# Kernel tuning notes

Hardware: AMD Instinct MI355X
Metric: run time of the kernel (lower is better)

## Reference

```python
import jax, jax.numpy as jnp
import numpy as np

P = 512       # person_attrs_dim
Z = 4096      # num_zones
T = 16384     # number of timesteps
E = 65536     # number of edges
PENALTY = 10.0


def setup_inputs() -> dict:
    key = jax.random.key(0)
    ks = jax.random.split(key, 10)
    person_attrs = jax.random.normal(ks[0], (P,), dtype=jnp.float32)
    times = jax.random.uniform(ks[1], (T,), dtype=jnp.float32)
    zone_features = jax.random.normal(ks[2], (Z, 16), dtype=jnp.float32)
    edge_index = jax.random.randint(ks[3], (2, E), 0, Z, dtype=jnp.int64)
    s = 0.05
    W1 = jax.random.normal(ks[4], (P + 1, 128), dtype=jnp.float32) * s
    b1 = jnp.zeros((128,), jnp.float32)
    W2 = jax.random.normal(ks[5], (128, 64), dtype=jnp.float32) * s
    b2 = jnp.zeros((64,), jnp.float32)
    W3 = jax.random.normal(ks[6], (64, Z), dtype=jnp.float32) * s
    b3 = jnp.zeros((Z,), jnp.float32)
    return {
        "person_attrs": person_attrs, "times": times,
        "zone_features": zone_features, "edge_index": edge_index,
        "W1": W1, "b1": b1, "W2": W2, "b2": b2, "W3": W3, "b3": b3,
    }


def reference(person_attrs, times, zone_features, edge_index, W1, b1, W2, b2, W3, b3):
    Zn = W3.shape[1]
    Tn = times.shape[0]

    # ---- set_graph_data: symmetric adjacency + self loops ----
    adj = jnp.zeros((Zn, Zn), jnp.float32)
    adj = adj.at[edge_index[0], edge_index[1]].set(1.0)
    adj = adj.at[edge_index[1], edge_index[0]].set(1.0)
    diag = jnp.arange(Zn)
    adj = adj.at[diag, diag].set(1.0)

    # ---- batched MLP over all timesteps (inputs don't depend on decode state) ----
    # input per step: concat(person_attrs, time)  -> [T, P+1]
    x = jnp.concatenate(
        [jnp.broadcast_to(person_attrs, (Tn, person_attrs.shape[0])), times[:, None]],
        axis=1,
    )
    h = jax.nn.relu(x @ W1 + b1)          # [T, 128]  (dropout is identity in eval)
    h = jax.nn.relu(h @ W2 + b2)          # [T, 64]
    raw = h @ W3 + b3                     # [T, Z]

    # ---- sequential graph-masked decode (training=True soft-penalty branch) ----
    def step(cur_zone, raw_t):
        constrained = raw_t - PENALTY * (1.0 - adj[cur_zone])  # [Z]
        nxt = jnp.argmax(constrained).astype(jnp.int32)
        return nxt, constrained

    _, zone_logits = jax.lax.scan(step, jnp.int32(0), raw)     # [T, Z]
    return zone_logits
```

## Files before the change

### kernel.cpp

```cpp
#include <hip/hip_runtime.h>
#include <hip/hip_bf16.h>
#include <stdint.h>

typedef uint16_t u16;
typedef uint32_t u32;
typedef uint64_t u64;
typedef unsigned char u8;

#define TT 16384
#define ZZ 4096
#define EE 65536
#define LBLK 32
#define NBLK 512
#define SUPW 16
#define NSUP 32
#define ADJ_STRIDE 80
#define UCAP 2048
#define PEN 10.0f

#define WS_BITS   0x000000
#define WS_GMKEY  0x200000
#define WS_DEG    0x220000
#define WS_ADJL   0x224000
#define WS_NCH    0x2C4000
#define WS_CVEC   0x2C5000
#define WS_WVEC   0x2C5200
#define WS_H2     0x2C5400
#define WS_M      WS_H2
#define WS_H      0x6C5400
#define WS_SB     0x705400
#define WS_CUR    0x705C00

__device__ __forceinline__ u64 mkkey(float v, u32 z) {
  u32 u = __float_as_uint(v);
  u32 sf = u ^ ((u32)((int)u >> 31) | 0x80000000u);
  return ((u64)sf << 12) | (u64)(4095u - z);
}
__device__ __forceinline__ float key_val(u64 k) {
  u32 sf = (u32)(k >> 12);
  u32 u = (sf & 0x80000000u) ? (sf ^ 0x80000000u) : ~sf;
  return __uint_as_float(u);
}

__device__ __forceinline__ u64 eval_part(int s, int part, const u64* keys, u64 gkey,
                                         const u16* adjl, int nc) {
  const u64* alq = (const u64*)(adjl + (size_t)s * ADJ_STRIDE) + part * 5;
  int cnt = nc - part * 5;
  u64 c0 = (cnt > 0) ? alq[0] : 0;
  u64 c1 = (cnt > 1) ? alq[1] : 0;
  u64 c2 = (cnt > 2) ? alq[2] : 0;
  u64 c3 = (cnt > 3) ? alq[3] : 0;
  u64 c4 = (cnt > 4) ? alq[4] : 0;
  u64 bb = gkey;
#define CM(cv, cnd) { u32 lo = (u32)(cv), hi = (u32)((cv) >> 32);                \
    u64 k0 = keys[lo & 0xFFFFu]; u64 k1 = keys[lo >> 16];                        \
    u64 k2 = keys[hi & 0xFFFFu]; u64 k3 = keys[hi >> 16];                        \
    u64 t01 = k0 > k1 ? k0 : k1; u64 t23 = k2 > k3 ? k2 : k3;                    \
    u64 tm = t01 > t23 ? t01 : t23;                                              \
    if ((cnd) && tm > bb) bb = tm; }
  CM(c0, cnt > 0) CM(c1, cnt > 1) CM(c2, cnt > 2) CM(c3, cnt > 3) CM(c4, cnt > 4)
#undef CM
  return bb;
}

__global__ __launch_bounds__(256) void k_setupA(u32* bits, u32* deg, u16* adjl,
                                                const float* pa, const float* W1,
                                                const float* b1,
                                                float* cvec, float* wvec) {
  __shared__ float pal[512];
  int tid = threadIdx.x;
  if (blockIdx.x < 16) {
    int z = blockIdx.x * 256 + tid;
    bits[(size_t)z * 128 + (z >> 5)] = 1u << (z & 31);
    deg[z] = 1;
    adjl[(size_t)z * ADJ_STRIDE] = (u16)z;
    return;
  }
  for (int i = tid; i < 512; i += 256) pal[i] = pa[i];
  __syncthreads();
  if (tid < 128) {
    float acc = b1[tid];
    for (int i = 0; i < 512; i++) acc = fmaf(pal[i], W1[(size_t)i * 128 + tid], acc);
    cvec[tid] = acc;
    wvec[tid] = W1[512 * 128 + tid];
  }
}

__global__ void k_edges(const int* ei, u32* bits, u32* deg, u16* adjl) {
  int e = blockIdx.x * blockDim.x + threadIdx.x;
  if (e >= EE) return;
  int u = ei[e], v = ei[EE + e];
#pragma unroll
  for (int dir = 0; dir < 2; dir++) {
    int a = dir ? v : u, b = dir ? u : v;
    u32 bit = 1u << (b & 31);
    u32 old = atomicOr(&bits[(size_t)a * 128 + (b >> 5)], bit);
    if (!(old & bit)) {
      u32 p = atomicAdd(&deg[a], 1u);
      if (p < ADJ_STRIDE) adjl[(size_t)a * ADJ_STRIDE + p] = (u16)b;
    }
  }
}

__global__ __launch_bounds__(256) void k_setupC(const u32* deg, u16* adjl, u8* nchp,
                                                const float* times, const float* W2,
                                                const float* b2, const float* cvec,
                                                const float* wvec, float* h2) {
  __shared__ float W2T[64][132];
  __shared__ float h1b[4][128];
  __shared__ float cl[128], wl[128], b2l[64];
  int tid = threadIdx.x;
  if (blockIdx.x < 16) {
    int z = blockIdx.x * 256 + tid;
    int d = (int)deg[z]; if (d > ADJ_STRIDE) d = ADJ_STRIDE;
    int dp = (d + 3) & ~3;
    for (int k = d; k < dp; k++) adjl[(size_t)z * ADJ_STRIDE + k] = (u16)z;
    nchp[z] = (u8)(dp >> 2);
    return;
  }
  for (int idx = tid; idx < 128 * 64; idx += 256) {
    int i = idx >> 6, j = idx & 63;
    W2T[j][i] = W2[idx];
  }
  if (tid < 128) { cl[tid] = cvec[tid]; wl[tid] = wvec[tid]; }
  else if (tid < 192) b2l[tid - 128] = b2[tid - 128];
  __syncthreads();
  int w = tid >> 6, lane = tid & 63;
  int t = (blockIdx.x - 16) * 4 + w;
  float tv = times[t];
  h1b[w][lane]      = fmaxf(fmaf(tv, wl[lane],      cl[lane]),      0.f);
  h1b[w][lane + 64] = fmaxf(fmaf(tv, wl[lane + 64], cl[lane + 64]), 0.f);
  __syncthreads();
  float acc = b2l[lane];
  const float4* hr = (const float4*)&h1b[w][0];
  const float4* Wr = (const float4*)&W2T[lane][0];
#pragma unroll
  for (int i4 = 0; i4 < 32; i4++) {
    float4 a = hr[i4], bb = Wr[i4];
    acc += a.x * bb.x; acc += a.y * bb.y; acc += a.z * bb.z; acc += a.w * bb.w;
  }
  acc = fmaxf(acc, 0.f);
  h2[(size_t)t * 64 + lane] = acc;
}

__global__ __launch_bounds__(256) void k_raw(const float* h2, const float* W3,
                                             const float* b3, float* out,
                                             u64* gmkey) {
  __shared__ float w3t[64][128];
  __shared__ float h2t[64][72];
  int tid = threadIdx.x;
  int zblk = blockIdx.x & 31, tblk = blockIdx.x >> 5;
  int z0 = zblk * 128, t0 = tblk * 64;
#pragma unroll
  for (int it = 0; it < 8; it++) {
    int f4 = tid + it * 256;
    int k = f4 >> 5, jj = (f4 & 31) * 4;
    *(float4*)&w3t[k][jj] = *(const float4*)(W3 + (size_t)k * ZZ + z0 + jj);
  }
#pragma unroll
  for (int it = 0; it < 4; it++) {
    int f4 = tid + it * 256;
    int r = f4 >> 4, kk = (f4 & 15) * 4;
    float4 h = *(const float4*)(h2 + (size_t)(t0 + r) * 64 + kk);
    h2t[kk + 0][r] = h.x; h2t[kk + 1][r] = h.y;
    h2t[kk + 2][r] = h.z; h2t[kk + 3][r] = h.w;
  }
  __syncthreads();
  int zq = tid & 31, tq = tid >> 5;
  float4 acc[8];
#pragma unroll
  for (int r = 0; r < 8; r++) acc[r] = make_float4(0.f, 0.f, 0.f, 0.f);
  for (int k = 0; k < 64; k++) {
    float4 w = *(const float4*)&w3t[k][zq * 4];
    float4 hA = *(const float4*)&h2t[k][tq * 8];
    float4 hB = *(const float4*)&h2t[k][tq * 8 + 4];
    acc[0].x += hA.x * w.x; acc[0].y += hA.x * w.y; acc[0].z += hA.x * w.z; acc[0].w += hA.x * w.w;
    acc[1].x += hA.y * w.x; acc[1].y += hA.y * w.y; acc[1].z += hA.y * w.z; acc[1].w += hA.y * w.w;
    acc[2].x += hA.z * w.x; acc[2].y += hA.z * w.y; acc[2].z += hA.z * w.z; acc[2].w += hA.z * w.w;
    acc[3].x += hA.w * w.x; acc[3].y += hA.w * w.y; acc[3].z += hA.w * w.z; acc[3].w += hA.w * w.w;
    acc[4].x += hB.x * w.x; acc[4].y += hB.x * w.y; acc[4].z += hB.x * w.z; acc[4].w += hB.x * w.w;
    acc[5].x += hB.y * w.x; acc[5].y += hB.y * w.y; acc[5].z += hB.y * w.z; acc[5].w += hB.y * w.w;
    acc[6].x += hB.z * w.x; acc[6].y += hB.z * w.y; acc[6].z += hB.z * w.z; acc[6].w += hB.z * w.w;
    acc[7].x += hB.w * w.x; acc[7].y += hB.w * w.y; acc[7].z += hB.w * w.z; acc[7].w += hB.w * w.w;
  }
  int z = z0 + zq * 4;
  float4 b3v = *(const float4*)(b3 + z);
  int lane = tid & 63;
  int half = lane >> 5;
#pragma unroll
  for (int r = 0; r < 8; r++) {
    int t = t0 + tq * 8 + r;
    float4 v;
    v.x = acc[r].x + b3v.x - PEN; v.y = acc[r].y + b3v.y - PEN;
    v.z = acc[r].z + b3v.z - PEN; v.w = acc[r].w + b3v.w - PEN;
    *(float4*)(out + (size_t)t * ZZ + z) = v;
    float lv = v.x; u32 lz = (u32)z;
    if (v.y > lv) { lv = v.y; lz = (u32)(z + 1); }
    if (v.z > lv) { lv = v.z; lz = (u32)(z + 2); }
    if (v.w > lv) { lv = v.w; lz = (u32)(z + 3); }
    float mv = lv;
#pragma unroll
    for (int off = 16; off >= 1; off >>= 1) {
      float o = __shfl_xor(mv, off);
      mv = o > mv ? o : mv;
    }
    u64 msk = __ballot(lv == mv);
    u32 hm = (u32)(msk >> (half * 32));
    int fl = __ffs(hm) - 1 + half * 32;
    u32 zbest = __shfl(lz, fl);
    if ((lane & 31) == 0)
      atomicMax((unsigned long long*)&gmkey[t], (unsigned long long)mkkey(mv, zbest));
  }
}

__global__ __launch_bounds__(512) void k_stage1(const float* raw, const u16* adjl,
                                                const u8* nchp, const u64* gmkey,
                                                u16* M) {
  __shared__ u64 keys[ZZ];
  __shared__ u16 I[ZZ];
  __shared__ u16 ev[ZZ];
  __shared__ u16 U[2][UCAP];
  __shared__ u8  nchl[ZZ];
  __shared__ u32 markw[128];
  __shared__ u32 mcnt2[2];
  __shared__ u64 gmk[LBLK];
  int tid = threadIdx.x;
  int b = blockIdx.x, t0 = b * LBLK;
  *(u64*)&nchl[tid * 8] = *(const u64*)(nchp + tid * 8);
  if (tid < LBLK) gmk[tid] = gmkey[t0 + tid];
  {
    const float4* src = (const float4*)(raw + (size_t)t0 * ZZ);
    float4 r0 = src[tid], r1 = src[tid + 512];
    int z0 = tid * 4;
    keys[z0 + 0] = mkkey(r0.x, z0 + 0);
    keys[z0 + 1] = mkkey(r0.y, z0 + 1);
    keys[z0 + 2] = mkkey(r0.z, z0 + 2);
    keys[z0 + 3] = mkkey(r0.w, z0 + 3);
    int z1 = (tid + 512) * 4;
    keys[z1 + 0] = mkkey(r1.x, z1 + 0);
    keys[z1 + 1] = mkkey(r1.y, z1 + 1);
    keys[z1 + 2] = mkkey(r1.z, z1 + 2);
    keys[z1 + 3] = mkkey(r1.w, z1 + 3);
  }
  __syncthreads();
  int lane = tid & 63;
  u64 lmask = (((u64)1) << lane) - 1ull;
  int part = tid & 3;
  int m = ZZ, pb = 0;
  bool dense = true;
  for (int i = 0; i < LBLK; i++) {
    int t = t0 + i;
    int tn = t + 1; if (tn > TT - 1) tn = TT - 1;
    const float4* srcn = (const float4*)(raw + (size_t)tn * ZZ);
    float4 p0 = srcn[tid], p1 = srcn[tid + 512];
    if (tid < 128) markw[tid] = 0;
    if (tid == 128) mcnt2[pb ^ 1] = 0;
    u64 gk = gmk[i];
    float gv = key_val(gk) - PEN;
    u32 gi = 4095u - (u32)(gk & 0xFFFu);
    u64 gkey = mkkey(gv, gi);
    int m4 = m << 2;
    for (int u = tid; u < m4; u += 512) {
      int s = dense ? (u >> 2) : (int)U[pb][u >> 2];
      u64 pk = eval_part(s, part, keys, gkey, adjl, (int)nchl[s]);
      u64 o1 = __shfl_xor(pk, 1); pk = o1 > pk ? o1 : pk;
      u64 o2 = __shfl_xor(pk, 2); pk = o2 > pk ? o2 : pk;
      if (part == 0) ev[s] = (u16)(4095u - ((u32)pk & 0xFFFu));
    }
    __syncthreads();
    if (i == 0) {
#pragma unroll
      for (int q = 0; q < 8; q++) {
        int j = tid + q * 512;
        I[j] = ev[j];
      }
    } else {
#pragma unroll
      for (int q = 0; q < 8; q++) {
        int j = tid + q * 512;
        I[j] = ev[I[j]];
      }
    }
    for (int u = tid; u < m; u += 512) {
      int s = dense ? u : (int)U[pb][u];
      u32 ns = ev[s];
      u32 wi = ns >> 5, bit = 1u << (ns & 31);
      u32 old = atomicOr(&markw[wi], bit);
      bool isnew = !(old & bit);
      u64 msk = __ballot(isnew ? 1 : 0);
      u32 base = 0;
      if (lane == 0) base = msk ? atomicAdd(&mcnt2[pb ^ 1], (u32)__popcll(msk)) : 0u;
      base = __shfl(base, 0);
      if (isnew) {
        u32 idx = base + (u32)__popcll(msk & lmask);
        if (idx < UCAP) U[pb ^ 1][idx] = (u16)ns;
      }
    }
    {
      int z0 = tid * 4;
      keys[z0 + 0] = mkkey(p0.x, z0 + 0);
      keys[z0 + 1] = mkkey(p0.y, z0 + 1);
      keys[z0 + 2] = mkkey(p0.z, z0 + 2);
      keys[z0 + 3] = mkkey(p0.w, z0 + 3);
      int z1 = (tid + 512) * 4;
      keys[z1 + 0] = mkkey(p1.x, z1 + 0);
      keys[z1 + 1] = mkkey(p1.y, z1 + 1);
      keys[z1 + 2] = mkkey(p1.z, z1 + 2);
      keys[z1 + 3] = mkkey(p1.w, z1 + 3);
    }
    __syncthreads();
    m = (int)mcnt2[pb ^ 1];
    dense = (m > UCAP);
    if (dense) m = ZZ;
    pb ^= 1;
  }
  {
    u64* md = (u64*)(M + (size_t)b * ZZ);
    md[tid * 2]     = *(const u64*)&I[tid * 8];
    md[tid * 2 + 1] = *(const u64*)&I[tid * 8 + 4];
  }
}

__global__ __launch_bounds__(256) void k_super(const u16* G, u16* H) {
  int g = blockIdx.x, tid = threadIdx.x;
  u32 v[16];
#pragma unroll
  for (int q = 0; q < 16; q++) v[q] = G[(size_t)(g * SUPW) * ZZ + tid + q * 256];
  for (int k = 1; k < SUPW; k++) {
    const u16* Gk = G + (size_t)(g * SUPW + k) * ZZ;
#pragma unroll
    for (int q = 0; q < 16; q++) v[q] = Gk[v[q]];
  }
#pragma unroll
  for (int q = 0; q < 16; q++) H[(size_t)g * ZZ + tid + q * 256] = (u16)v[q];
}

__global__ void k_chase(const u16* G, const u16* H, u32* sb) {
  __shared__ u32 ug[NSUP];
  int tid = threadIdx.x;
  if (tid == 0) {
    u32 s = 0;
    for (int g = 0; g < NSUP; g++) { ug[g] = s; s = H[(size_t)g * ZZ + s]; }
  }
  __syncthreads();
  if (tid < NSUP) {
    u32 s = ug[tid];
    for (int k = 0; k < SUPW; k++) {
      int b = tid * SUPW + k;
      sb[b] = s;
      s = G[(size_t)b * ZZ + s];
    }
  }
}

__global__ __launch_bounds__(64) void k_replay2(const float* out, const u16* adjl,
                                                const u8* nchp, const u64* gmkey,
                                                const u32* sb, u32* curz) {
  int b = blockIdx.x, t0 = b * LBLK;
  int lane = threadIdx.x;
  u32 s = sb[b];
  for (int i = 0; i < LBLK; i++) {
    int t = t0 + i;
    if (lane == 0) curz[t] = s;
    u64 gk = gmkey[t];
    float gv = key_val(gk) - PEN;
    u32 gi = 4095u - (u32)(gk & 0xFFFu);
    int dp = ((int)nchp[s]) << 2;
    const u16* al = adjl + (size_t)s * ADJ_STRIDE;
    const float* r = out + (size_t)t * ZZ;
    float bv = gv; u32 bi = gi;
    if (lane < dp) {
      u32 nb = al[lane]; float v = r[nb];
      if (v > bv || (v == bv && nb < bi)) { bv = v; bi = nb; }
    }
    if (lane + 64 < dp) {
      u32 nb = al[lane + 64]; float v = r[nb];
      if (v > bv || (v == bv && nb < bi)) { bv = v; bi = nb; }
    }
#pragma unroll
    for (int off = 32; off >= 1; off >>= 1) {
      float ov = __shfl_xor(bv, off);
      u32 oi  = __shfl_xor(bi, off);
      if (ov > bv || (ov == bv && oi < bi)) { bv = ov; bi = oi; }
    }
    s = bi;
  }
}

__global__ __launch_bounds__(256) void k_out2(float* out, const u32* curz, const u32* bits) {
  int t = blockIdx.x * 4 + (threadIdx.x >> 6);
  int lane = threadIdx.x & 63;
  u32 c = curz[t];
  u64 w = ((const u64*)(bits + (size_t)c * 128))[lane];
  float* p = out + (size_t)t * ZZ + lane * 64;
  while (w) {
    int bpos = __ffsll((unsigned long long)w) - 1;
    p[bpos] += PEN;
    w &= w - 1;
  }
}

extern "C" void kernel_launch(void* const* d_in, const int* in_sizes, int n_in,
                              void* d_out, int out_size, void* d_ws, size_t ws_size,
                              hipStream_t stream) {
  const float* pa    = (const float*)d_in[0];
  const float* times = (const float*)d_in[1];
  const int*   ei    = (const int*)d_in[3];
  const float* W1    = (const float*)d_in[4];
  const float* b1    = (const float*)d_in[5];
  const float* W2    = (const float*)d_in[6];
  const float* b2    = (const float*)d_in[7];
  const float* W3    = (const float*)d_in[8];
  const float* b3    = (const float*)d_in[9];
  float* out = (float*)d_out;
  char* ws = (char*)d_ws;

  u32* bits = (u32*)(ws + WS_BITS);
  u64* gmkey = (u64*)(ws + WS_GMKEY);
  u32* deg  = (u32*)(ws + WS_DEG);
  u16* adjl = (u16*)(ws + WS_ADJL);
  u8*  nchp = (u8*)(ws + WS_NCH);
  float* cvec = (float*)(ws + WS_CVEC);
  float* wvec = (float*)(ws + WS_WVEC);
  float* h2   = (float*)(ws + WS_H2);
  u16* M = (u16*)(ws + WS_M);
  u16* H = (u16*)(ws + WS_H);
  u32* sb   = (u32*)(ws + WS_SB);
  u32* curz = (u32*)(ws + WS_CUR);

  hipMemsetAsync(ws, 0, 0x220000, stream);
  hipLaunchKernelGGL(k_setupA, dim3(17), dim3(256), 0, stream,
                     bits, deg, adjl, pa, W1, b1, cvec, wvec);
  hipLaunchKernelGGL(k_edges, dim3(EE / 256), dim3(256), 0, stream, ei, bits, deg, adjl);
  hipLaunchKernelGGL(k_setupC, dim3(16 + TT / 4), dim3(256), 0, stream,
                     deg, adjl, nchp, times, W2, b2, cvec, wvec, h2);
  hipLaunchKernelGGL(k_raw, dim3(8192), dim3(256), 0, stream, h2, W3, b3, out, gmkey);
  hipLaunchKernelGGL(k_stage1, dim3(NBLK), dim3(512), 0, stream, out, adjl, nchp, gmkey, M);
  hipLaunchKernelGGL(k_super, dim3(NSUP), dim3(256), 0, stream, M, H);
  hipLaunchKernelGGL(k_chase, dim3(1), dim3(64), 0, stream, M, H, sb);
  hipLaunchKernelGGL(k_replay2, dim3(NBLK), dim3(64), 0, stream, out, adjl, nchp, gmkey, sb, curz);
  hipLaunchKernelGGL(k_out2, dim3(TT / 4), dim3(256), 0, stream, out, curz, bits);
}
```

Measured before the change: 442.1 us.

## Shrink stage1 shared keys to 32-bit, interleave adjacency reads, fuse output fixup into replay

Stage1 now stores 32-bit sign-flipped float keys in shared memory instead of 64-bit packed keys and rebuilds the index tiebreak on the fly. This halves LDS footprint and traffic, and lets each key row be written with a single vectorized uint4 store. Adjacency chunk reads are interleaved across the four part-lanes for more coalesced access. The separate k_out2 penalty-fixup kernel is folded into k_replay2, removing one launch and the curz global round trip. The trade-off is that the fixup now runs on only 512 blocks of 64 threads instead of 4096 blocks of 256.

```diff
diff --git a/kernel.cpp b/kernel.cpp
--- a/kernel.cpp
+++ b/kernel.cpp
@@ -29,12 +29,13 @@
 #define WS_M      WS_H2
 #define WS_H      0x6C5400
 #define WS_SB     0x705400
-#define WS_CUR    0x705C00
-
+
+__device__ __forceinline__ u32 sfu(float v) {
+  u32 u = __float_as_uint(v);
+  return u ^ ((u32)((int)u >> 31) | 0x80000000u);
+}
 __device__ __forceinline__ u64 mkkey(float v, u32 z) {
-  u32 u = __float_as_uint(v);
-  u32 sf = u ^ ((u32)((int)u >> 31) | 0x80000000u);
-  return ((u64)sf << 12) | (u64)(4095u - z);
+  return ((u64)sfu(v) << 12) | (u64)(4095u - z);
 }
 __device__ __forceinline__ float key_val(u64 k) {
   u32 sf = (u32)(k >> 12);
@@ -42,23 +43,27 @@
   return __uint_as_float(u);
 }
 
-__device__ __forceinline__ u64 eval_part(int s, int part, const u64* keys, u64 gkey,
+__device__ __forceinline__ u64 eval_part(int s, int part, const u32* keys, u64 gkey,
                                          const u16* adjl, int nc) {
-  const u64* alq = (const u64*)(adjl + (size_t)s * ADJ_STRIDE) + part * 5;
-  int cnt = nc - part * 5;
-  u64 c0 = (cnt > 0) ? alq[0] : 0;
-  u64 c1 = (cnt > 1) ? alq[1] : 0;
-  u64 c2 = (cnt > 2) ? alq[2] : 0;
-  u64 c3 = (cnt > 3) ? alq[3] : 0;
-  u64 c4 = (cnt > 4) ? alq[4] : 0;
+  const u64* alq = (const u64*)(adjl + (size_t)s * ADJ_STRIDE);
+  u64 c0 = (part      < nc) ? alq[part]      : 0;
+  u64 c1 = (part + 4  < nc) ? alq[part + 4]  : 0;
+  u64 c2 = (part + 8  < nc) ? alq[part + 8]  : 0;
+  u64 c3 = (part + 12 < nc) ? alq[part + 12] : 0;
+  u64 c4 = (part + 16 < nc) ? alq[part + 16] : 0;
   u64 bb = gkey;
-#define CM(cv, cnd) { u32 lo = (u32)(cv), hi = (u32)((cv) >> 32);                \
-    u64 k0 = keys[lo & 0xFFFFu]; u64 k1 = keys[lo >> 16];                        \
-    u64 k2 = keys[hi & 0xFFFFu]; u64 k3 = keys[hi >> 16];                        \
+#define CM(cv, cnd) if (cnd) {                                                   \
+    u32 lo = (u32)(cv), hi = (u32)((cv) >> 32);                                  \
+    u32 za = lo & 0xFFFFu, zb = lo >> 16, zc = hi & 0xFFFFu, zd = hi >> 16;      \
+    u64 k0 = ((u64)keys[za] << 32) | (u64)(za ^ 0xFFFu);                         \
+    u64 k1 = ((u64)keys[zb] << 32) | (u64)(zb ^ 0xFFFu);                         \
+    u64 k2 = ((u64)keys[zc] << 32) | (u64)(zc ^ 0xFFFu);                         \
+    u64 k3 = ((u64)keys[zd] << 32) | (u64)(zd ^ 0xFFFu);                         \
     u64 t01 = k0 > k1 ? k0 : k1; u64 t23 = k2 > k3 ? k2 : k3;                    \
     u64 tm = t01 > t23 ? t01 : t23;                                              \
-    if ((cnd) && tm > bb) bb = tm; }
-  CM(c0, cnt > 0) CM(c1, cnt > 1) CM(c2, cnt > 2) CM(c3, cnt > 3) CM(c4, cnt > 4)
+    bb = tm > bb ? tm : bb; }
+  CM(c0, part < nc) CM(c1, part + 4 < nc) CM(c2, part + 8 < nc)
+  CM(c3, part + 12 < nc) CM(c4, part + 16 < nc)
 #undef CM
   return bb;
 }
@@ -216,7 +221,7 @@
 __global__ __launch_bounds__(512) void k_stage1(const float* raw, const u16* adjl,
                                                 const u8* nchp, const u64* gmkey,
                                                 u16* M) {
-  __shared__ u64 keys[ZZ];
+  __shared__ u32 keys[ZZ];
   __shared__ u16 I[ZZ];
   __shared__ u16 ev[ZZ];
   __shared__ u16 U[2][UCAP];
@@ -231,16 +236,8 @@
   {
     const float4* src = (const float4*)(raw + (size_t)t0 * ZZ);
     float4 r0 = src[tid], r1 = src[tid + 512];
-    int z0 = tid * 4;
-    keys[z0 + 0] = mkkey(r0.x, z0 + 0);
-    keys[z0 + 1] = mkkey(r0.y, z0 + 1);
-    keys[z0 + 2] = mkkey(r0.z, z0 + 2);
-    keys[z0 + 3] = mkkey(r0.w, z0 + 3);
-    int z1 = (tid + 512) * 4;
-    keys[z1 + 0] = mkkey(r1.x, z1 + 0);
-    keys[z1 + 1] = mkkey(r1.y, z1 + 1);
-    keys[z1 + 2] = mkkey(r1.z, z1 + 2);
-    keys[z1 + 3] = mkkey(r1.w, z1 + 3);
+    ((uint4*)keys)[tid]       = make_uint4(sfu(r0.x), sfu(r0.y), sfu(r0.z), sfu(r0.w));
+    ((uint4*)keys)[tid + 512] = make_uint4(sfu(r1.x), sfu(r1.y), sfu(r1.z), sfu(r1.w));
   }
   __syncthreads();
   int lane = tid & 63;
@@ -257,8 +254,7 @@
     if (tid == 128) mcnt2[pb ^ 1] = 0;
     u64 gk = gmk[i];
     float gv = key_val(gk) - PEN;
-    u32 gi = 4095u - (u32)(gk & 0xFFFu);
-    u64 gkey = mkkey(gv, gi);
+    u64 gkey = ((u64)sfu(gv) << 32) | (u64)(gk & 0xFFFu);
     int m4 = m << 2;
     for (int u = tid; u < m4; u += 512) {
       int s = dense ? (u >> 2) : (int)U[pb][u >> 2];
@@ -296,18 +292,8 @@
         if (idx < UCAP) U[pb ^ 1][idx] = (u16)ns;
       }
     }
-    {
-      int z0 = tid * 4;
-      keys[z0 + 0] = mkkey(p0.x, z0 + 0);
-      keys[z0 + 1] = mkkey(p0.y, z0 + 1);
-      keys[z0 + 2] = mkkey(p0.z, z0 + 2);
-      keys[z0 + 3] = mkkey(p0.w, z0 + 3);
-      int z1 = (tid + 512) * 4;
-      keys[z1 + 0] = mkkey(p1.x, z1 + 0);
-      keys[z1 + 1] = mkkey(p1.y, z1 + 1);
-      keys[z1 + 2] = mkkey(p1.z, z1 + 2);
-      keys[z1 + 3] = mkkey(p1.w, z1 + 3);
-    }
+    ((uint4*)keys)[tid]       = make_uint4(sfu(p0.x), sfu(p0.y), sfu(p0.z), sfu(p0.w));
+    ((uint4*)keys)[tid + 512] = make_uint4(sfu(p1.x), sfu(p1.y), sfu(p1.z), sfu(p1.w));
     __syncthreads();
     m = (int)mcnt2[pb ^ 1];
     dense = (m > UCAP);
@@ -353,15 +339,16 @@
   }
 }
 
-__global__ __launch_bounds__(64) void k_replay2(const float* out, const u16* adjl,
+__global__ __launch_bounds__(64) void k_replay2(float* out, const u16* adjl,
                                                 const u8* nchp, const u64* gmkey,
-                                                const u32* sb, u32* curz) {
+                                                const u32* sb, const u32* bits) {
+  __shared__ u32 curl[LBLK];
   int b = blockIdx.x, t0 = b * LBLK;
   int lane = threadIdx.x;
   u32 s = sb[b];
   for (int i = 0; i < LBLK; i++) {
     int t = t0 + i;
-    if (lane == 0) curz[t] = s;
+    if (lane == 0) curl[i] = s;
     u64 gk = gmkey[t];
     float gv = key_val(gk) - PEN;
     u32 gi = 4095u - (u32)(gk & 0xFFFu);
@@ -385,18 +372,17 @@
     }
     s = bi;
   }
-}
-
-__global__ __launch_bounds__(256) void k_out2(float* out, const u32* curz, const u32* bits) {
-  int t = blockIdx.x * 4 + (threadIdx.x >> 6);
-  int lane = threadIdx.x & 63;
-  u32 c = curz[t];
-  u64 w = ((const u64*)(bits + (size_t)c * 128))[lane];
-  float* p = out + (size_t)t * ZZ + lane * 64;
-  while (w) {
-    int bpos = __ffsll((unsigned long long)w) - 1;
-    p[bpos] += PEN;
-    w &= w - 1;
+  __syncthreads();
+  for (int i = 0; i < LBLK; i++) {
+    int t = t0 + i;
+    u32 c = curl[i];
+    u64 w = ((const u64*)(bits + (size_t)c * 128))[lane];
+    float* p = out + (size_t)t * ZZ + lane * 64;
+    while (w) {
+      int bp = __ffsll((unsigned long long)w) - 1;
+      p[bp] += PEN;
+      w &= w - 1;
+    }
   }
 }
 
@@ -426,7 +412,6 @@
   u16* M = (u16*)(ws + WS_M);
   u16* H = (u16*)(ws + WS_H);
   u32* sb   = (u32*)(ws + WS_SB);
-  u32* curz = (u32*)(ws + WS_CUR);
 
   hipMemsetAsync(ws, 0, 0x220000, stream);
   hipLaunchKernelGGL(k_setupA, dim3(17), dim3(256), 0, stream,
@@ -438,6 +423,5 @@
   hipLaunchKernelGGL(k_stage1, dim3(NBLK), dim3(512), 0, stream, out, adjl, nchp, gmkey, M);
   hipLaunchKernelGGL(k_super, dim3(NSUP), dim3(256), 0, stream, M, H);
   hipLaunchKernelGGL(k_chase, dim3(1), dim3(64), 0, stream, M, H, sb);
-  hipLaunchKernelGGL(k_replay2, dim3(NBLK), dim3(64), 0, stream, out, adjl, nchp, gmkey, sb, curz);
-  hipLaunchKernelGGL(k_out2, dim3(TT / 4), dim3(256), 0, stream, out, curz, bits);
-}
+  hipLaunchKernelGGL(k_replay2, dim3(NBLK), dim3(64), 0, stream, out, adjl, nchp, gmkey, sb, bits);
+}
```

After: 456.5 us. +3.3%, slower.
